# Kernel optimization log

Measured on AMD Instinct MI355X. Metric: run time of the kernel, lower is better.

The kernel has to match this reference:

```python
import jax, jax.numpy as jnp
import numpy as np

EPS = 1e-5

def _rms(t, w):
    # RMSNorm over last dim with learned scale w (broadcastable)
    return t * jax.lax.rsqrt(jnp.mean(t * t, axis=-1, keepdims=True) + EPS) * w

def setup_inputs() -> dict:
    key = jax.random.key(0)
    ks = jax.random.split(key, 8)
    B, S, D, H, HD, M = 2, 2048, 1024, 16, 64, 2
    E = H * HD
    sc = 0.02
    x = jax.random.normal(ks[0], (B, S, D), jnp.float32)
    attn_mask = jnp.zeros((S, S), jnp.float32)  # additive mask
    mod_ids = jax.random.randint(ks[1], (B, S), 0, M)
    Wq = jax.random.normal(ks[2], (M, D, E), jnp.float32) * sc
    Wk = jax.random.normal(ks[3], (M, D, E), jnp.float32) * sc
    Wv = jax.random.normal(ks[4], (M, D, E), jnp.float32) * sc
    Wo = jax.random.normal(ks[5], (M, E, D), jnp.float32) * sc
    qn_w = jnp.ones((M, HD), jnp.float32)
    kn_w = jnp.ones((M, HD), jnp.float32)
    attn_norm_w = jnp.ones((M, D), jnp.float32)
    return {"x": x, "attn_mask": attn_mask, "mod_ids": mod_ids,
            "Wq": Wq, "Wk": Wk, "Wv": Wv, "Wo": Wo,
            "qn_w": qn_w, "kn_w": kn_w, "attn_norm_w": attn_norm_w}

def reference(x, attn_mask, mod_ids, Wq, Wk, Wv, Wo, qn_w, kn_w, attn_norm_w):
    B, S, D = x.shape
    M = Wq.shape[0]
    HD = qn_w.shape[-1]
    E = Wq.shape[-1]
    H = E // HD
    msk = jax.nn.one_hot(mod_ids, M, dtype=x.dtype)  # [B,S,M] one-hot routing

    # modality-expert QKV projections: [M,B,S,E]
    q_m = jnp.einsum('bsd,mde->mbse', x, Wq).reshape(M, B, S, H, HD)
    k_m = jnp.einsum('bsd,mde->mbse', x, Wk).reshape(M, B, S, H, HD)
    v_m = jnp.einsum('bsd,mde->mbse', x, Wv)
    # per-modality, per-head QK RMSNorm
    q_m = _rms(q_m, qn_w[:, None, None, None, :]).reshape(M, B, S, E)
    k_m = _rms(k_m, kn_w[:, None, None, None, :]).reshape(M, B, S, E)

    # merge modalities (scatter by routing mask)
    q = jnp.einsum('bsm,mbse->bse', msk, q_m).reshape(B, S, H, HD)
    k = jnp.einsum('bsm,mbse->bse', msk, k_m).reshape(B, S, H, HD)
    v = jnp.einsum('bsm,mbse->bse', msk, v_m).reshape(B, S, H, HD)

    # standard multi-head attention
    scores = jnp.einsum('bqhd,bkhd->bhqk', q, k) / jnp.sqrt(jnp.asarray(HD, x.dtype))
    scores = scores + attn_mask  # additive mask broadcast over [B,H]
    attn = jax.nn.softmax(scores, axis=-1)
    ctx = jnp.einsum('bhqk,bkhd->bqhd', attn, v).reshape(B, S, E)
    attn_weights = attn.mean(axis=1)  # [B,S,S], averaged over heads

    # modality-expert output projection + RMSNorm, scatter-merge back
    o_m = jnp.einsum('bse,med->mbsd', ctx, Wo)
    o_m = _rms(o_m, attn_norm_w[:, None, None, :])
    out = jnp.einsum('bsm,mbsd->bsd', msk, o_m)
    return out, attn_weights
```

## Files before the change

kernel.cpp:

```cpp
#include <hip/hip_runtime.h>
#include <cstdint>

#define Bc  2
#define Sc  2048
#define Dc  1024
#define Ec  1024
#define Hc  16
#define HDc 64
#define TTc (Bc*Sc)
#define TILE_R 128
#define NTILES 36
#define EPSc 1e-5f
#define LOG2E 1.44269504f
#define C2    (0.125f*LOG2E)

typedef unsigned short u16;
using bf8   = __attribute__((ext_vector_type(8))) short;
using f32x4 = __attribute__((ext_vector_type(4))) float;
#define MFMA(a,b,c) __builtin_amdgcn_mfma_f32_16x16x32_bf16(a,b,c,0,0,0)

static __device__ __forceinline__ u16 f2b(float f){
    return (u16)((__float_as_uint(f) + 0x8000u) >> 16);
}
static __device__ __forceinline__ float b2f(u16 s){
    return __uint_as_float(((unsigned)s) << 16);
}
static __device__ __forceinline__ float ex2(float x){
    return __builtin_amdgcn_exp2f(x);
}
static __device__ __forceinline__ unsigned cvtpk(float a, float b){
    unsigned r;
    asm("v_cvt_pk_bf16_f32 %0, %1, %2" : "=v"(r) : "v"(a), "v"(b));
    return r;
}
union bfpack { unsigned u[4]; bf8 v; };
static __device__ __forceinline__ float max3f(float a, float b, float c){
    return fmaxf(fmaxf(a, b), c);
}
static __device__ __forceinline__ u16* swz(u16* base, int row, int col8){
    return base + row*64 + ((col8 ^ (row & 7)) << 3);
}
static __device__ __forceinline__ const u16* swzc(const u16* base, int row, int col8){
    return base + row*64 + ((col8 ^ (row & 7)) << 3);
}
typedef const __attribute__((address_space(1))) void* gp1;
typedef __attribute__((address_space(3))) void* lp3;
static __device__ __forceinline__ void gl16(const void* g, void* l){
    __builtin_amdgcn_global_load_lds((gp1)g, (lp3)l, 16, 0, 0);
}
static __device__ __forceinline__ int pinv(int lr){
    return (lr & 0x23) | ((lr & 0x10) >> 2) | ((lr & 0x0C) << 1);
}

__global__ void k_perm(const int* __restrict__ mod, int* __restrict__ perm,
                       int* __restrict__ tmeta, u16* __restrict__ zbuf)
{
    __shared__ int cnt[4], segstart[4];
    int t = threadIdx.x;
    for (int i = t; i < 2048; i += 256) zbuf[i] = 0;
    if (t < 4) cnt[t] = 0;
    __syncthreads();
    for (int i = t; i < TTc; i += 256){
        int b = i >> 11; int m = mod[i];
        atomicAdd(&cnt[b*2+m], 1);
    }
    __syncthreads();
    if (t == 0){
        int off = 0;
        for (int i = 0; i < 4; i++){
            segstart[i] = off;
            int pad = ((cnt[i] + TILE_R - 1)/TILE_R)*TILE_R;
            for (int tt = off/TILE_R; tt < (off+pad)/TILE_R; tt++) tmeta[tt] = i;
            off += pad;
        }
        for (int tt = off/TILE_R; tt < NTILES; tt++) tmeta[tt] = -1;
    }
    __syncthreads();
    if (t < 4) cnt[t] = 0;
    for (int i = t; i < NTILES*TILE_R; i += 256) perm[i] = -1;
    __syncthreads();
    for (int i = t; i < TTc; i += 256){
        int b = i >> 11, s = i & 2047; int m = mod[i];
        int r = atomicAdd(&cnt[b*2+m], 1);
        perm[segstart[b*2+m] + r] = s;
    }
}

__global__ __launch_bounds__(256) void k_prep(
    const float* __restrict__ x, const float* __restrict__ mask,
    u16* __restrict__ xb, u16* __restrict__ maskb)
{
    int bid = blockIdx.x;
    if (bid < 4096){
        int i = (bid*256 + threadIdx.x)*4;
        float4 v = *(const float4*)&x[i];
        ushort4 o;
        o.x = f2b(v.x); o.y = f2b(v.y); o.z = f2b(v.z); o.w = f2b(v.w);
        *(ushort4*)&xb[i] = o;
    } else {
        int i = ((bid-4096)*256 + threadIdx.x)*4;
        float4 v = *(const float4*)&mask[i];
        ushort4 o;
        o.x = f2b(v.x*LOG2E); o.y = f2b(v.y*LOG2E);
        o.z = f2b(v.z*LOG2E); o.w = f2b(v.w*LOG2E);
        *(ushort4*)&maskb[i] = o;
    }
}

__global__ __launch_bounds__(256) void k_tcvt(
    const float* __restrict__ s0, const float* __restrict__ s1,
    const float* __restrict__ s2, const float* __restrict__ s3,
    u16* __restrict__ d0, u16* __restrict__ d1,
    u16* __restrict__ d2, u16* __restrict__ d3)
{
    int wsel = blockIdx.z >> 1, m = blockIdx.z & 1;
    const float* src = (wsel==0?s0:wsel==1?s1:wsel==2?s2:s3) + (size_t)m*1048576;
    u16*       dst = (wsel==0?d0:wsel==1?d1:wsel==2?d2:d3) + (size_t)m*1048576;
    __shared__ float sh[32][33];
    int t = threadIdx.x;
    int i0 = blockIdx.x*32, j0 = blockIdx.y*32;
    {
        int i = t >> 3, j4 = (t & 7)*4;
        *(float4*)&sh[i][j4] = *(const float4*)&src[(size_t)(i0+i)*1024 + j0 + j4];
    }
    __syncthreads();
    {
        int j = t >> 3, i4 = (t & 7)*4;
        ushort4 o;
        o.x = f2b(sh[i4+0][j]); o.y = f2b(sh[i4+1][j]);
        o.z = f2b(sh[i4+2][j]); o.w = f2b(sh[i4+3][j]);
        *(ushort4*)&dst[(size_t)(j0+j)*1024 + i0 + i4] = o;
    }
}

__global__ __launch_bounds__(256) void k_qkv(
    const u16* __restrict__ xb, const u16* __restrict__ wqT,
    const u16* __restrict__ wkT, const u16* __restrict__ wvT,
    const int* __restrict__ perm, const int* __restrict__ tmeta,
    const float* __restrict__ qnw, const float* __restrict__ knw,
    const u16* __restrict__ zbuf,
    u16* __restrict__ qb, u16* __restrict__ kb, u16* __restrict__ vb)
{
    int meta = tmeta[blockIdx.y];
    if (meta < 0) return;
    int b = meta >> 1, m = meta & 1;
    const u16* W = (blockIdx.z==0 ? wqT : (blockIdx.z==1 ? wkT : wvT)) + (size_t)m*Ec*Dc;
    u16* outp    = (blockIdx.z==0 ? qb  : (blockIdx.z==1 ? kb  : vb));
    int c0 = blockIdx.x*128;
    int t = threadIdx.x, lane = t & 63, wv_ = t >> 6;
    int quad = lane >> 4, lc = lane & 15;

    __shared__ u16 at[128*64];
    __shared__ u16 bt[128*64];
    __shared__ int sperm[128];
    if (t < 128) sperm[t] = perm[blockIdx.y*128 + t];
    f32x4 acc[2][8];
    #pragma unroll
    for (int i=0;i<2;i++)
        #pragma unroll
        for (int j=0;j<8;j++) acc[i][j] = (f32x4){0.f,0.f,0.f,0.f};
    __syncthreads();

    int colsw = ((lane & 7) ^ (lane >> 3)) << 3;
    const u16* ab[4]; const u16* bb[4];
    #pragma unroll
    for (int i = 0; i < 4; i++){
        int row = wv_*32 + i*8 + (lane >> 3);
        int s_ = sperm[row];
        ab[i] = (s_ >= 0) ? (xb + ((size_t)(b*Sc + s_))*Dc + colsw) : zbuf;
        bb[i] = W + (size_t)(c0 + row)*Dc + colsw;
    }

    for (int d0 = 0; d0 < Dc; d0 += 64){
        #pragma unroll
        for (int i = 0; i < 4; i++){
            gl16(ab[i] + d0, &at[(wv_*4 + i)*512]);
            gl16(bb[i] + d0, &bt[(wv_*4 + i)*512]);
        }
        __syncthreads();
        #pragma unroll
        for (int ks = 0; ks < 2; ks++){
            bf8 a0 = *(const bf8*)swzc(at, wv_*32 + lc,      ks*4 + quad);
            bf8 a1 = *(const bf8*)swzc(at, wv_*32 + 16 + lc, ks*4 + quad);
            #pragma unroll
            for (int nb = 0; nb < 8; nb++){
                bf8 bb2 = *(const bf8*)swzc(bt, nb*16 + lc, ks*4 + quad);
                acc[0][nb] = MFMA(a0, bb2, acc[0][nb]);
                acc[1][nb] = MFMA(a1, bb2, acc[1][nb]);
            }
        }
        __syncthreads();
    }

    if (blockIdx.z < 2){
        const float* nw = (blockIdx.z==0 ? qnw : knw) + m*HDc;
        float cs = (blockIdx.z==0) ? C2 : 1.f;
        float w0 = nw[lc]*cs, w1 = nw[16+lc]*cs, w2 = nw[32+lc]*cs, w3 = nw[48+lc]*cs;
        #pragma unroll
        for (int mb = 0; mb < 2; mb++){
            #pragma unroll
            for (int r = 0; r < 4; r++){
                #pragma unroll
                for (int g = 0; g < 2; g++){
                    float ss = 0.f;
                    #pragma unroll
                    for (int j = 0; j < 4; j++){
                        float v2 = acc[mb][g*4+j][r];
                        ss += v2*v2;
                    }
                    ss += __shfl_xor(ss, 1, 64);
                    ss += __shfl_xor(ss, 2, 64);
                    ss += __shfl_xor(ss, 4, 64);
                    ss += __shfl_xor(ss, 8, 64);
                    float rs = rsqrtf(ss*(1.f/64.f) + EPSc);
                    acc[mb][g*4+0][r] *= rs*w0;
                    acc[mb][g*4+1][r] *= rs*w1;
                    acc[mb][g*4+2][r] *= rs*w2;
                    acc[mb][g*4+3][r] *= rs*w3;
                }
            }
        }
    }

    int h0 = c0 >> 6;
    #pragma unroll
    for (int mb = 0; mb < 2; mb++){
        #pragma unroll
        for (int r = 0; r < 4; r++){
            int row = wv_*32 + mb*16 + quad*4 + r;
            int s_ = sperm[row];
            if (s_ < 0) continue;
            #pragma unroll
            for (int nb = 0; nb < 8; nb++){
                int col = nb*16 + lc;
                int h = h0 + (col >> 6), hd = col & 63;
                outp[(((size_t)(b*Hc + h))*Sc + s_)*HDc + hd] = f2b(acc[mb][nb][r]);
            }
        }
    }
}

__global__ __launch_bounds__(256) void k_vt(const u16* __restrict__ vb,
                                            u16* __restrict__ vtb)
{
    __shared__ u16 sh[64][72];
    int t = threadIdx.x;
    int s0 = blockIdx.x*64, bh = blockIdx.y;
    {
        int rr = t >> 2, cc = (t & 3)*16;
        const u16* src = vb + ((size_t)bh*Sc + s0 + rr)*HDc + cc;
        *(uint4*)&sh[rr][cc]   = *(const uint4*)(src);
        *(uint4*)&sh[rr][cc+8] = *(const uint4*)(src+8);
    }
    __syncthreads();
    {
        int hd = t >> 2, sc = (t & 3)*16;
        u16 tmp[16];
        #pragma unroll
        for (int j = 0; j < 16; j++) tmp[j] = sh[sc+j][hd];
        u16* dst = vtb + ((size_t)bh*HDc + hd)*Sc + s0 + sc;
        *(uint4*)(dst)   = *(const uint4*)&tmp[0];
        *(uint4*)(dst+8) = *(const uint4*)&tmp[8];
    }
}

__global__ __launch_bounds__(256) void k_flash(
    const u16* __restrict__ qb, const u16* __restrict__ kb,
    const u16* __restrict__ vtb, const u16* __restrict__ maskb,
    float* __restrict__ lstc, u16* __restrict__ c0)
{
    int qs0 = blockIdx.x*64, h = blockIdx.y;
    int b = blockIdx.z;
    int t = threadIdx.x, lane = t & 63, wv_ = t >> 6;
    int quad = lane >> 4, lc = lane & 15;
    __shared__ u16 kt[2][64*64];
    __shared__ u16 vt[2][64*64];
    const u16* qp  = qb  + ((size_t)(b*Hc+h))*Sc*HDc;
    const u16* kp  = kb  + ((size_t)(b*Hc+h))*Sc*HDc;
    const u16* vtp = vtb + ((size_t)(b*Hc+h))*HDc*Sc;
    const u16* mq  = maskb + (size_t)(qs0 + wv_*16 + lc)*Sc;
    bf8 aq[2];
    #pragma unroll
    for (int ks = 0; ks < 2; ks++)
        aq[ks] = *(const bf8*)(qp + (size_t)(qs0 + wv_*16 + lc)*HDc + ks*32 + quad*8);
    bfpack onep; onep.u[0] = onep.u[1] = onep.u[2] = onep.u[3] = 0x3F803F80u;
    bf8 ones = onep.v;
    float rm = -1.0e30f;
    f32x4 racc = (f32x4){0.f,0.f,0.f,0.f};
    f32x4 oacc[4];
    #pragma unroll
    for (int j=0;j<4;j++) oacc[j] = (f32x4){0.f,0.f,0.f,0.f};

    int lsub = lane >> 3;
    int colsw = ((lane & 7) ^ lsub) << 3;
    int lrA = wv_*16 + lsub, lrB = wv_*16 + 8 + lsub;
    const u16* kg0 = kp + (size_t)pinv(lrA)*HDc + colsw;
    const u16* kg1 = kp + (size_t)pinv(lrB)*HDc + colsw;
    const u16* vg0 = vtp + (size_t)lrA*Sc + colsw;
    const u16* vg1 = vtp + (size_t)lrB*Sc + colsw;
    int kdo0 = (wv_*16 + 0)*64, kdo1 = (wv_*16 + 8)*64;

    gl16(kg0, &kt[0][kdo0]);
    gl16(kg1, &kt[0][kdo1]);
    gl16(vg0, &vt[0][kdo0]);
    gl16(vg1, &vt[0][kdo1]);
    ushort4 mv[2][2];
    #pragma unroll
    for (int a1 = 0; a1 < 2; a1++)
        #pragma unroll
        for (int b1 = 0; b1 < 2; b1++)
            mv[a1][b1] = *(const ushort4*)(mq + a1*32 + quad*8 + b1*4);
    __syncthreads();

    int cur = 0;
    for (int kc = 0; kc < Sc; kc += 64){
        int nxt = (kc + 64 < Sc) ? kc + 64 : kc;
        gl16(kg0 + (size_t)nxt*HDc, &kt[cur^1][kdo0]);
        gl16(kg1 + (size_t)nxt*HDc, &kt[cur^1][kdo1]);
        gl16(vg0 + nxt, &vt[cur^1][kdo0]);
        gl16(vg1 + nxt, &vt[cur^1][kdo1]);
        ushort4 mvn[2][2];
        #pragma unroll
        for (int a1 = 0; a1 < 2; a1++)
            #pragma unroll
            for (int b1 = 0; b1 < 2; b1++)
                mvn[a1][b1] = *(const ushort4*)(mq + nxt + a1*32 + quad*8 + b1*4);

        const u16* ktc = kt[cur];
        const u16* vtc = vt[cur];
        f32x4 acc[4];
        #pragma unroll
        for (int a1 = 0; a1 < 2; a1++){
            #pragma unroll
            for (int b1 = 0; b1 < 2; b1++){
                int nb = 2*a1 + b1;
                acc[nb][0] = b2f(mv[a1][b1].x);
                acc[nb][1] = b2f(mv[a1][b1].y);
                acc[nb][2] = b2f(mv[a1][b1].z);
                acc[nb][3] = b2f(mv[a1][b1].w);
            }
        }
        #pragma unroll
        for (int ks = 0; ks < 2; ks++){
            #pragma unroll
            for (int nb = 0; nb < 4; nb++){
                bf8 ak = *(const bf8*)swzc(ktc, nb*16 + lc, ks*4 + quad);
                acc[nb] = MFMA(ak, aq[ks], acc[nb]);
            }
        }
        float m0_ = max3f(acc[0][0], acc[0][1], acc[0][2]);
        float m1_ = max3f(acc[0][3], acc[1][0], acc[1][1]);
        float m2_ = max3f(acc[1][2], acc[1][3], acc[2][0]);
        float m3_ = max3f(acc[2][1], acc[2][2], acc[2][3]);
        float m4_ = max3f(acc[3][0], acc[3][1], acc[3][2]);
        float mxl = fmaxf(max3f(m0_, m1_, m2_), max3f(m3_, m4_, acc[3][3]));
        if (__any(mxl > rm + 8.f)){
            float mx = fmaxf(mxl, __shfl_xor(mxl, 16, 64));
            mx = fmaxf(mx, __shfl_xor(mx, 32, 64));
            float nm = fmaxf(rm, mx);
            float fac = ex2(rm - nm);
            rm = nm;
            float f0 = __shfl(fac, quad*4+0, 64);
            float f1 = __shfl(fac, quad*4+1, 64);
            float f2 = __shfl(fac, quad*4+2, 64);
            float f3 = __shfl(fac, quad*4+3, 64);
            racc[0] *= f0; racc[1] *= f1; racc[2] *= f2; racc[3] *= f3;
            #pragma unroll
            for (int nb = 0; nb < 4; nb++){
                oacc[nb][0] *= f0; oacc[nb][1] *= f1;
                oacc[nb][2] *= f2; oacc[nb][3] *= f3;
            }
        }
        #pragma unroll
        for (int a1 = 0; a1 < 2; a1++){
            bfpack pk;
            pk.u[0] = cvtpk(ex2(acc[2*a1][0] - rm),   ex2(acc[2*a1][1] - rm));
            pk.u[1] = cvtpk(ex2(acc[2*a1][2] - rm),   ex2(acc[2*a1][3] - rm));
            pk.u[2] = cvtpk(ex2(acc[2*a1+1][0] - rm), ex2(acc[2*a1+1][1] - rm));
            pk.u[3] = cvtpk(ex2(acc[2*a1+1][2] - rm), ex2(acc[2*a1+1][3] - rm));
            bf8 ap = pk.v;
            racc = MFMA(ap, ones, racc);
            #pragma unroll
            for (int nb2 = 0; nb2 < 4; nb2++){
                bf8 bv = *(const bf8*)swzc(vtc, nb2*16 + lc, a1*4 + quad);
                oacc[nb2] = MFMA(ap, bv, oacc[nb2]);
            }
        }
        __syncthreads();
        #pragma unroll
        for (int a1 = 0; a1 < 2; a1++)
            #pragma unroll
            for (int b1 = 0; b1 < 2; b1++)
                mv[a1][b1] = mvn[a1][b1];
        cur ^= 1;
    }
    float rmr[4];
    #pragma unroll
    for (int r = 0; r < 4; r++) rmr[r] = __shfl(rm, quad*4 + r, 64);
    size_t sbase = ((size_t)(b*Hc+h))*Sc + qs0 + wv_*16;
    if (lc == 0){
        #pragma unroll
        for (int r = 0; r < 4; r++)
            lstc[sbase + quad*4 + r] = rmr[r] + log2f(racc[r]);
    }
    #pragma unroll
    for (int r = 0; r < 4; r++){
        float ir = 1.f/racc[r];
        int tok = qs0 + wv_*16 + quad*4 + r;
        #pragma unroll
        for (int nb = 0; nb < 4; nb++){
            int hd = nb*16 + lc;
            c0[((size_t)(b*Sc + tok))*Ec + h*HDc + hd] = f2b(oacc[nb][r]*ir);
        }
    }
}

__global__ __launch_bounds__(256) void k_attnw(
    const u16* __restrict__ qb, const u16* __restrict__ kb,
    const u16* __restrict__ maskb, const float* __restrict__ lstc,
    float* __restrict__ awout)
{
    int qs0 = blockIdx.x*64, ks0 = blockIdx.y*64, b = blockIdx.z;
    int t = threadIdx.x, lane = t & 63, wv_ = t >> 6;
    int quad = lane >> 4, lc = lane & 15;
    __shared__ u16 kt[64*64];
    __shared__ float scc[64];
    f32x4 T[4];
    #pragma unroll
    for (int j=0;j<4;j++) T[j] = (f32x4){0.f,0.f,0.f,0.f};

    int lsub = lane >> 3;
    int colsw = ((lane & 7) ^ lsub) << 3;
    int lrA = wv_*16 + lsub, lrB = wv_*16 + 8 + lsub;
    u16* kd0 = &kt[(wv_*16 + 0)*64];
    u16* kd1 = &kt[(wv_*16 + 8)*64];

    for (int h = 0; h < Hc; h++){
        __syncthreads();
        const u16* qp = qb + ((size_t)(b*Hc+h))*Sc*HDc;
        const u16* kp = kb + ((size_t)(b*Hc+h))*Sc*HDc;
        bf8 aq[2];
        #pragma unroll
        for (int ks = 0; ks < 2; ks++)
            aq[ks] = *(const bf8*)(qp + (size_t)(qs0 + wv_*16 + lc)*HDc + ks*32 + quad*8);
        gl16(kp + (size_t)(ks0 + lrA)*HDc + colsw, kd0);
        gl16(kp + (size_t)(ks0 + lrB)*HDc + colsw, kd1);
        if (t < 64)
            scc[t] = -lstc[((size_t)(b*Hc+h))*Sc + qs0 + t];
        __syncthreads();
        f32x4 minit = *(const f32x4*)&scc[wv_*16 + quad*4];
        f32x4 acc[4];
        #pragma unroll
        for (int j=0;j<4;j++) acc[j] = minit;
        #pragma unroll
        for (int ks = 0; ks < 2; ks++){
            #pragma unroll
            for (int nb = 0; nb < 4; nb++){
                bf8 bb = *(const bf8*)swzc(kt, nb*16 + lc, ks*4 + quad);
                acc[nb] = MFMA(aq[ks], bb, acc[nb]);
            }
        }
        #pragma unroll
        for (int r = 0; r < 4; r++){
            #pragma unroll
            for (int nb = 0; nb < 4; nb++)
                T[nb][r] += ex2(acc[nb][r]);
        }
    }
    #pragma unroll
    for (int r = 0; r < 4; r++){
        int gq = qs0 + wv_*16 + quad*4 + r;
        #pragma unroll
        for (int nb = 0; nb < 4; nb++){
            int gk = ks0 + nb*16 + lc;
            float mk = b2f(maskb[(size_t)gq*Sc + gk]);
            awout[(size_t)b*Sc*Sc + (size_t)gq*Sc + gk]
                = T[nb][r]*ex2(mk)*(1.f/16.f);
        }
    }
}

__global__ __launch_bounds__(256) void k_oproj(
    const u16* __restrict__ ctxb, const u16* __restrict__ woT,
    const int* __restrict__ perm, const int* __restrict__ tmeta,
    const u16* __restrict__ zbuf, float* __restrict__ opre)
{
    int meta = tmeta[blockIdx.y];
    if (meta < 0) return;
    int b = meta >> 1, m = meta & 1;
    const u16* W = woT + (size_t)m*Ec*Dc;
    int c0 = blockIdx.x*128;
    int t = threadIdx.x, lane = t & 63, wv_ = t >> 6;
    int quad = lane >> 4, lc = lane & 15;
    __shared__ u16 at[128*64];
    __shared__ u16 bt[128*64];
    __shared__ int sperm[128];
    if (t < 128) sperm[t] = perm[blockIdx.y*128 + t];
    f32x4 acc[2][8];
    #pragma unroll
    for (int i=0;i<2;i++)
        #pragma unroll
        for (int j=0;j<8;j++) acc[i][j] = (f32x4){0.f,0.f,0.f,0.f};
    __syncthreads();

    int colsw = ((lane & 7) ^ (lane >> 3)) << 3;
    const u16* ab[4]; const u16* bb[4];
    #pragma unroll
    for (int i = 0; i < 4; i++){
        int row = wv_*32 + i*8 + (lane >> 3);
        int s_ = sperm[row];
        ab[i] = (s_ >= 0) ? (ctxb + ((size_t)(b*Sc + s_))*Ec + colsw) : zbuf;
        bb[i] = W + (size_t)(c0 + row)*Ec + colsw;
    }

    for (int d0 = 0; d0 < Ec; d0 += 64){
        #pragma unroll
        for (int i = 0; i < 4; i++){
            gl16(ab[i] + d0, &at[(wv_*4 + i)*512]);
            gl16(bb[i] + d0, &bt[(wv_*4 + i)*512]);
        }
        __syncthreads();
        #pragma unroll
        for (int ks = 0; ks < 2; ks++){
            bf8 a0 = *(const bf8*)swzc(at, wv_*32 + lc,      ks*4 + quad);
            bf8 a1 = *(const bf8*)swzc(at, wv_*32 + 16 + lc, ks*4 + quad);
            #pragma unroll
            for (int nb = 0; nb < 8; nb++){
                bf8 bb2 = *(const bf8*)swzc(bt, nb*16 + lc, ks*4 + quad);
                acc[0][nb] = MFMA(a0, bb2, acc[0][nb]);
                acc[1][nb] = MFMA(a1, bb2, acc[1][nb]);
            }
        }
        __syncthreads();
    }
    #pragma unroll
    for (int mb = 0; mb < 2; mb++){
        #pragma unroll
        for (int r = 0; r < 4; r++){
            int row = wv_*32 + mb*16 + quad*4 + r;
            int s_ = sperm[row];
            if (s_ < 0) continue;
            #pragma unroll
            for (int nb = 0; nb < 8; nb++){
                int col = c0 + nb*16 + lc;
                opre[((size_t)(b*Sc + s_))*Dc + col] = acc[mb][nb][r];
            }
        }
    }
}

__global__ __launch_bounds__(256) void k_onorm(
    const float* __restrict__ opre, const float* __restrict__ anw,
    const int* __restrict__ mod, float* __restrict__ out)
{
    int row = blockIdx.x;
    int m = mod[row];
    int t = threadIdx.x;
    float val[4];
    float ss = 0.f;
    #pragma unroll
    for (int j=0;j<4;j++){
        val[j] = opre[(size_t)row*Dc + t + 256*j];
        ss += val[j]*val[j];
    }
    #pragma unroll
    for (int o=32;o>0;o>>=1) ss += __shfl_xor(ss, o, 64);
    __shared__ float red[4];
    int wid = t>>6, lane = t&63;
    if (lane==0) red[wid]=ss;
    __syncthreads();
    float tot = red[0]+red[1]+red[2]+red[3];
    float rms = rsqrtf(tot*(1.f/1024.f) + EPSc);
    #pragma unroll
    for (int j=0;j<4;j++)
        out[(size_t)row*Dc + t + 256*j] = val[j]*rms*anw[m*Dc + t + 256*j];
}

extern "C" void kernel_launch(void* const* d_in, const int* in_sizes, int n_in,
                              void* d_out, int out_size, void* d_ws, size_t ws_size,
                              hipStream_t stream)
{
    const float* x    = (const float*)d_in[0];
    const float* mask = (const float*)d_in[1];
    const int*   mod  = (const int*)  d_in[2];
    const float* Wq   = (const float*)d_in[3];
    const float* Wk   = (const float*)d_in[4];
    const float* Wv   = (const float*)d_in[5];
    const float* Wo   = (const float*)d_in[6];
    const float* qnw  = (const float*)d_in[7];
    const float* knw  = (const float*)d_in[8];
    const float* anw  = (const float*)d_in[9];

    float* out   = (float*)d_out;
    float* awout = out + (size_t)Bc*Sc*Dc;

    float* ws = (float*)d_ws;
    u16* qb    = (u16*)(ws + 0);
    u16* kb    = (u16*)(ws + 2097152);
    u16* vb    = (u16*)(ws + 4194304);
    u16* xb    = (u16*)(ws + 6291456);
    u16* ctx0  = xb;
    u16* vtb   = (u16*)(ws + 8388608);
    u16* wqT   = (u16*)(ws + 10485760);
    u16* wkT   = (u16*)(ws + 11534336);
    u16* wvT   = (u16*)(ws + 12582912);
    u16* woT   = (u16*)(ws + 13631488);
    float* lstc= ws + 14680064;
    u16* maskb = (u16*)(ws + 15335424);
    int* perm  = (int*)(ws + 17432576);
    int* tmeta = perm + NTILES*TILE_R;
    u16* zbuf  = (u16*)(tmeta + NTILES + 28);
    float* opre = ws;

    k_perm  <<<dim3(1),            256, 0, stream>>>(mod, perm, tmeta, zbuf);
    k_prep  <<<dim3(8192),         256, 0, stream>>>(x, mask, xb, maskb);
    k_tcvt  <<<dim3(32,32,8),      256, 0, stream>>>(Wq, Wk, Wv, Wo, wqT, wkT, wvT, woT);
    k_qkv   <<<dim3(8,NTILES,3),   256, 0, stream>>>(xb, wqT, wkT, wvT, perm, tmeta,
                                                     qnw, knw, zbuf, qb, kb, vb);
    k_vt    <<<dim3(32,32),        256, 0, stream>>>(vb, vtb);
    k_flash <<<dim3(32,16,2),      256, 0, stream>>>(qb, kb, vtb, maskb, lstc, ctx0);
    k_attnw <<<dim3(32,32,2),      256, 0, stream>>>(qb, kb, maskb, lstc, awout);
    k_oproj <<<dim3(8,NTILES),     256, 0, stream>>>(ctx0, woT, perm, tmeta, zbuf, opre);
    k_onorm <<<dim3(4096),         256, 0, stream>>>(opre, anw, mod, out);
}
```

Before: 337.5 us.

## Merge preprocessing kernels into one launch and widen attention-weight key tile

Three preprocessing kernels (routing permutation, x/mask bf16 conversion, weight transpose-convert) become one launch that dispatches on block index, removing two launch gaps and the serial single-block permutation stage. The attention-weights kernel now covers 128 keys per block instead of 64, so each Q fragment load and log-sum-exp fetch is reused across twice as many keys and the grid is halved. The trade-off is more accumulator registers (8 f32x4 tiles) and fewer blocks, which may reduce occupancy. The lone permutation block now runs last in the fused grid and can form a tail.

```diff
diff --git a/kernel.cpp b/kernel.cpp
--- a/kernel.cpp
+++ b/kernel.cpp
@@ -52,84 +52,80 @@
     return (lr & 0x23) | ((lr & 0x10) >> 2) | ((lr & 0x0C) << 1);
 }
 
-__global__ void k_perm(const int* __restrict__ mod, int* __restrict__ perm,
-                       int* __restrict__ tmeta, u16* __restrict__ zbuf)
-{
-    __shared__ int cnt[4], segstart[4];
+__global__ __launch_bounds__(256) void k_pre(
+    const float* __restrict__ x, const float* __restrict__ mask,
+    const int* __restrict__ mod,
+    const float* __restrict__ s0, const float* __restrict__ s1,
+    const float* __restrict__ s2, const float* __restrict__ s3,
+    u16* __restrict__ xb, u16* __restrict__ maskb,
+    u16* __restrict__ d0, u16* __restrict__ d1,
+    u16* __restrict__ d2, u16* __restrict__ d3,
+    int* __restrict__ perm, int* __restrict__ tmeta, u16* __restrict__ zbuf)
+{
+    int bid = blockIdx.x;
     int t = threadIdx.x;
-    for (int i = t; i < 2048; i += 256) zbuf[i] = 0;
-    if (t < 4) cnt[t] = 0;
-    __syncthreads();
-    for (int i = t; i < TTc; i += 256){
-        int b = i >> 11; int m = mod[i];
-        atomicAdd(&cnt[b*2+m], 1);
-    }
-    __syncthreads();
-    if (t == 0){
-        int off = 0;
-        for (int i = 0; i < 4; i++){
-            segstart[i] = off;
-            int pad = ((cnt[i] + TILE_R - 1)/TILE_R)*TILE_R;
-            for (int tt = off/TILE_R; tt < (off+pad)/TILE_R; tt++) tmeta[tt] = i;
-            off += pad;
-        }
-        for (int tt = off/TILE_R; tt < NTILES; tt++) tmeta[tt] = -1;
-    }
-    __syncthreads();
-    if (t < 4) cnt[t] = 0;
-    for (int i = t; i < NTILES*TILE_R; i += 256) perm[i] = -1;
-    __syncthreads();
-    for (int i = t; i < TTc; i += 256){
-        int b = i >> 11, s = i & 2047; int m = mod[i];
-        int r = atomicAdd(&cnt[b*2+m], 1);
-        perm[segstart[b*2+m] + r] = s;
-    }
-}
-
-__global__ __launch_bounds__(256) void k_prep(
-    const float* __restrict__ x, const float* __restrict__ mask,
-    u16* __restrict__ xb, u16* __restrict__ maskb)
-{
-    int bid = blockIdx.x;
     if (bid < 4096){
-        int i = (bid*256 + threadIdx.x)*4;
+        int i = (bid*256 + t)*4;
         float4 v = *(const float4*)&x[i];
         ushort4 o;
         o.x = f2b(v.x); o.y = f2b(v.y); o.z = f2b(v.z); o.w = f2b(v.w);
         *(ushort4*)&xb[i] = o;
-    } else {
-        int i = ((bid-4096)*256 + threadIdx.x)*4;
+    } else if (bid < 8192){
+        int i = ((bid-4096)*256 + t)*4;
         float4 v = *(const float4*)&mask[i];
         ushort4 o;
         o.x = f2b(v.x*LOG2E); o.y = f2b(v.y*LOG2E);
         o.z = f2b(v.z*LOG2E); o.w = f2b(v.w*LOG2E);
         *(ushort4*)&maskb[i] = o;
-    }
-}
-
-__global__ __launch_bounds__(256) void k_tcvt(
-    const float* __restrict__ s0, const float* __restrict__ s1,
-    const float* __restrict__ s2, const float* __restrict__ s3,
-    u16* __restrict__ d0, u16* __restrict__ d1,
-    u16* __restrict__ d2, u16* __restrict__ d3)
-{
-    int wsel = blockIdx.z >> 1, m = blockIdx.z & 1;
-    const float* src = (wsel==0?s0:wsel==1?s1:wsel==2?s2:s3) + (size_t)m*1048576;
-    u16*       dst = (wsel==0?d0:wsel==1?d1:wsel==2?d2:d3) + (size_t)m*1048576;
-    __shared__ float sh[32][33];
-    int t = threadIdx.x;
-    int i0 = blockIdx.x*32, j0 = blockIdx.y*32;
-    {
-        int i = t >> 3, j4 = (t & 7)*4;
-        *(float4*)&sh[i][j4] = *(const float4*)&src[(size_t)(i0+i)*1024 + j0 + j4];
-    }
-    __syncthreads();
-    {
-        int j = t >> 3, i4 = (t & 7)*4;
-        ushort4 o;
-        o.x = f2b(sh[i4+0][j]); o.y = f2b(sh[i4+1][j]);
-        o.z = f2b(sh[i4+2][j]); o.w = f2b(sh[i4+3][j]);
-        *(ushort4*)&dst[(size_t)(j0+j)*1024 + i0 + i4] = o;
+    } else if (bid < 16384){
+        int id = bid - 8192;
+        int z = id >> 10, xy = id & 1023;
+        int wsel = z >> 1, m = z & 1;
+        const float* src = (wsel==0?s0:wsel==1?s1:wsel==2?s2:s3) + (size_t)m*1048576;
+        u16*       dst = (wsel==0?d0:wsel==1?d1:wsel==2?d2:d3) + (size_t)m*1048576;
+        __shared__ float sh[32][33];
+        int i0 = (xy & 31)*32, j0 = (xy >> 5)*32;
+        {
+            int i = t >> 3, j4 = (t & 7)*4;
+            *(float4*)&sh[i][j4] = *(const float4*)&src[(size_t)(i0+i)*1024 + j0 + j4];
+        }
+        __syncthreads();
+        {
+            int j = t >> 3, i4 = (t & 7)*4;
+            ushort4 o;
+            o.x = f2b(sh[i4+0][j]); o.y = f2b(sh[i4+1][j]);
+            o.z = f2b(sh[i4+2][j]); o.w = f2b(sh[i4+3][j]);
+            *(ushort4*)&dst[(size_t)(j0+j)*1024 + i0 + i4] = o;
+        }
+    } else {
+        __shared__ int cnt[4], segstart[4];
+        for (int i = t; i < 2048; i += 256) zbuf[i] = 0;
+        if (t < 4) cnt[t] = 0;
+        __syncthreads();
+        for (int i = t; i < TTc; i += 256){
+            int b = i >> 11; int m = mod[i];
+            atomicAdd(&cnt[b*2+m], 1);
+        }
+        __syncthreads();
+        if (t == 0){
+            int off = 0;
+            for (int i = 0; i < 4; i++){
+                segstart[i] = off;
+                int pad = ((cnt[i] + TILE_R - 1)/TILE_R)*TILE_R;
+                for (int tt = off/TILE_R; tt < (off+pad)/TILE_R; tt++) tmeta[tt] = i;
+                off += pad;
+            }
+            for (int tt = off/TILE_R; tt < NTILES; tt++) tmeta[tt] = -1;
+        }
+        __syncthreads();
+        if (t < 4) cnt[t] = 0;
+        for (int i = t; i < NTILES*TILE_R; i += 256) perm[i] = -1;
+        __syncthreads();
+        for (int i = t; i < TTc; i += 256){
+            int b = i >> 11, s = i & 2047; int m = mod[i];
+            int r = atomicAdd(&cnt[b*2+m], 1);
+            perm[segstart[b*2+m] + r] = s;
+        }
     }
 }
 
@@ -420,20 +416,17 @@
     const u16* __restrict__ maskb, const float* __restrict__ lstc,
     float* __restrict__ awout)
 {
-    int qs0 = blockIdx.x*64, ks0 = blockIdx.y*64, b = blockIdx.z;
+    int qs0 = blockIdx.x*64, ks0 = blockIdx.y*128, b = blockIdx.z;
     int t = threadIdx.x, lane = t & 63, wv_ = t >> 6;
     int quad = lane >> 4, lc = lane & 15;
-    __shared__ u16 kt[64*64];
+    __shared__ u16 kt[128*64];
     __shared__ float scc[64];
-    f32x4 T[4];
-    #pragma unroll
-    for (int j=0;j<4;j++) T[j] = (f32x4){0.f,0.f,0.f,0.f};
+    f32x4 T[8];
+    #pragma unroll
+    for (int j=0;j<8;j++) T[j] = (f32x4){0.f,0.f,0.f,0.f};
 
     int lsub = lane >> 3;
     int colsw = ((lane & 7) ^ lsub) << 3;
-    int lrA = wv_*16 + lsub, lrB = wv_*16 + 8 + lsub;
-    u16* kd0 = &kt[(wv_*16 + 0)*64];
-    u16* kd1 = &kt[(wv_*16 + 8)*64];
 
     for (int h = 0; h < Hc; h++){
         __syncthreads();
@@ -443,19 +436,22 @@
         #pragma unroll
         for (int ks = 0; ks < 2; ks++)
             aq[ks] = *(const bf8*)(qp + (size_t)(qs0 + wv_*16 + lc)*HDc + ks*32 + quad*8);
-        gl16(kp + (size_t)(ks0 + lrA)*HDc + colsw, kd0);
-        gl16(kp + (size_t)(ks0 + lrB)*HDc + colsw, kd1);
+        #pragma unroll
+        for (int i = 0; i < 4; i++){
+            int lr = wv_*32 + i*8 + lsub;
+            gl16(kp + (size_t)(ks0 + lr)*HDc + colsw, &kt[(wv_*32 + i*8)*64]);
+        }
         if (t < 64)
             scc[t] = -lstc[((size_t)(b*Hc+h))*Sc + qs0 + t];
         __syncthreads();
         f32x4 minit = *(const f32x4*)&scc[wv_*16 + quad*4];
-        f32x4 acc[4];
-        #pragma unroll
-        for (int j=0;j<4;j++) acc[j] = minit;
+        f32x4 acc[8];
+        #pragma unroll
+        for (int j=0;j<8;j++) acc[j] = minit;
         #pragma unroll
         for (int ks = 0; ks < 2; ks++){
             #pragma unroll
-            for (int nb = 0; nb < 4; nb++){
+            for (int nb = 0; nb < 8; nb++){
                 bf8 bb = *(const bf8*)swzc(kt, nb*16 + lc, ks*4 + quad);
                 acc[nb] = MFMA(aq[ks], bb, acc[nb]);
             }
@@ -463,7 +459,7 @@
         #pragma unroll
         for (int r = 0; r < 4; r++){
             #pragma unroll
-            for (int nb = 0; nb < 4; nb++)
+            for (int nb = 0; nb < 8; nb++)
                 T[nb][r] += ex2(acc[nb][r]);
         }
     }
@@ -471,7 +467,7 @@
     for (int r = 0; r < 4; r++){
         int gq = qs0 + wv_*16 + quad*4 + r;
         #pragma unroll
-        for (int nb = 0; nb < 4; nb++){
+        for (int nb = 0; nb < 8; nb++){
             int gk = ks0 + nb*16 + lc;
             float mk = b2f(maskb[(size_t)gq*Sc + gk]);
             awout[(size_t)b*Sc*Sc + (size_t)gq*Sc + gk]
@@ -612,14 +608,14 @@
     u16* zbuf  = (u16*)(tmeta + NTILES + 28);
     float* opre = ws;
 
-    k_perm  <<<dim3(1),            256, 0, stream>>>(mod, perm, tmeta, zbuf);
-    k_prep  <<<dim3(8192),         256, 0, stream>>>(x, mask, xb, maskb);
-    k_tcvt  <<<dim3(32,32,8),      256, 0, stream>>>(Wq, Wk, Wv, Wo, wqT, wkT, wvT, woT);
+    k_pre   <<<dim3(16385),        256, 0, stream>>>(x, mask, mod, Wq, Wk, Wv, Wo,
+                                                     xb, maskb, wqT, wkT, wvT, woT,
+                                                     perm, tmeta, zbuf);
     k_qkv   <<<dim3(8,NTILES,3),   256, 0, stream>>>(xb, wqT, wkT, wvT, perm, tmeta,
                                                      qnw, knw, zbuf, qb, kb, vb);
     k_vt    <<<dim3(32,32),        256, 0, stream>>>(vb, vtb);
     k_flash <<<dim3(32,16,2),      256, 0, stream>>>(qb, kb, vtb, maskb, lstc, ctx0);
-    k_attnw <<<dim3(32,32,2),      256, 0, stream>>>(qb, kb, maskb, lstc, awout);
+    k_attnw <<<dim3(32,16,2),      256, 0, stream>>>(qb, kb, maskb, lstc, awout);
     k_oproj <<<dim3(8,NTILES),     256, 0, stream>>>(ctx0, woT, perm, tmeta, zbuf, opre);
     k_onorm <<<dim3(4096),         256, 0, stream>>>(opre, anw, mod, out);
 }
```

Result: faster. 321.9 us (-4.6%).
